# Kernel tuning notes

Measured on AMD Instinct MI355X. Metric: run time of the kernel, lower is better.

## Reference

```python
import jax, jax.numpy as jnp
import numpy as np

NUM_GRAPHS = 64

def _sage(x, edge_index, Wl, bl, Wr):
    # PyG SAGEConv (mean aggr): out = lin_l(mean_{j in N(i)} x_j) + lin_r(x_i)
    src, dst = edge_index[0], edge_index[1]
    n = x.shape[0]
    summed = jax.ops.segment_sum(x[src], dst, num_segments=n)        # [N,F]
    deg = jax.ops.segment_sum(jnp.ones_like(src, dtype=x.dtype), dst, num_segments=n)
    agg = summed / jnp.maximum(deg, 1.0)[:, None]
    return agg @ Wl.T + bl + x @ Wr.T

def setup_inputs() -> dict:
    key = jax.random.key(0)
    ks = jax.random.split(key, 12)
    N, E, F, H = 50000, 600000, 128, 128
    x = jax.random.normal(ks[0], (N, F), dtype=jnp.float32)
    edge_index = jax.random.randint(ks[1], (2, E), 0, N, dtype=jnp.int64)
    batch = jnp.sort(jax.random.randint(ks[2], (N,), 0, NUM_GRAPHS, dtype=jnp.int64))
    s = lambda fan_in: 1.0 / np.sqrt(fan_in)
    return {
        "x": x, "edge_index": edge_index, "batch": batch,
        "W1l": jax.random.uniform(ks[3], (H, F), minval=-s(F), maxval=s(F)),
        "b1l": jnp.zeros((H,), jnp.float32),
        "W1r": jax.random.uniform(ks[4], (H, F), minval=-s(F), maxval=s(F)),
        "W2l": jax.random.uniform(ks[5], (H, H), minval=-s(H), maxval=s(H)),
        "b2l": jnp.zeros((H,), jnp.float32),
        "W2r": jax.random.uniform(ks[6], (H, H), minval=-s(H), maxval=s(H)),
        "Wc1": jax.random.uniform(ks[7], (H, H), minval=-s(H), maxval=s(H)),
        "bc1": jax.random.uniform(ks[8], (H,), minval=-s(H), maxval=s(H)),
        "Wc2": jax.random.uniform(ks[9], (1, H), minval=-s(H), maxval=s(H)),
        "bc2": jax.random.uniform(ks[10], (1,), minval=-s(H), maxval=s(H)),
    }

def reference(x, edge_index, batch, W1l, b1l, W1r, W2l, b2l, W2r, Wc1, bc1, Wc2, bc2):
    h = jax.nn.relu(_sage(x, edge_index, W1l, b1l, W1r))
    h = jax.nn.relu(_sage(h, edge_index, W2l, b2l, W2r))
    # global mean pool per graph
    gsum = jax.ops.segment_sum(h, batch, num_segments=NUM_GRAPHS)
    gcnt = jax.ops.segment_sum(jnp.ones((h.shape[0],), h.dtype), batch, num_segments=NUM_GRAPHS)
    gemb = gsum / jnp.maximum(gcnt, 1.0)[:, None]                    # [G,H]
    # classifier MLP (dropout = identity in eval)
    z = jax.nn.relu(gemb @ Wc1.T + bc1)
    out = (z @ Wc2.T + bc2).squeeze(-1)                              # [G]
    return out
```

## Files before the change

### kernel.cpp

```cpp
#include <hip/hip_runtime.h>


typedef __attribute__((ext_vector_type(8))) short bf16x8;
typedef __attribute__((ext_vector_type(8))) unsigned short ushort8;
typedef __attribute__((ext_vector_type(4))) float f32x4;

#define HBLK 4096

__device__ inline unsigned short f2bf(float f) {
  unsigned u = __float_as_uint(f);
  u += 0x7fff + ((u >> 16) & 1);
  return (unsigned short)(u >> 16);
}
__device__ inline float bf2f(unsigned short h) { return __uint_as_float(((unsigned)h) << 16); }


__device__ inline void wprep_body(int id, const float* __restrict__ Wl, const float* __restrict__ Wr,
                                  unsigned short* __restrict__ Bpre) {
  if (id >= 4096) return;
  int kk = id >> 9;
  int ct = (id >> 6) & 7;
  int l  = id & 63;
  int colIdx = ct * 16 + (l & 15);
  int k0 = kk * 32 + (l >> 4) * 8;
  const float* W = (k0 < 128) ? Wl : Wr;
  int kb = k0 & 127;
#pragma unroll
  for (int j = 0; j < 8; ++j) {
    float v = W[colIdx * 128 + kb + j];
    unsigned short h = f2bf(v);
    size_t bh = (size_t)kk * 8192 + ((size_t)ct * 64 + l) * 8 + j;
    Bpre[bh] = h;
    Bpre[bh + 4096] = f2bf(v - bf2f(h));
  }
}

__global__ __launch_bounds__(256) void k_prep(
    const float* __restrict__ x, unsigned short* __restrict__ xbf, int total,
    const float* __restrict__ W1l, const float* __restrict__ W1r, unsigned short* __restrict__ Bpre1,
    const float* __restrict__ W2l, const float* __restrict__ W2r, unsigned short* __restrict__ Bpre2,
    const int* __restrict__ batch, int* __restrict__ gcnt, float* __restrict__ gsum, int N,
    const int* __restrict__ ei, int* __restrict__ bhist, int E,
    int nTobf, int nEblk) {
  __shared__ int h[256];
  int b = blockIdx.x;
  int tid = threadIdx.x;
  if (b < nTobf) {
    int i = (b * 256 + tid) * 4;
    if (i + 3 < total) {
      float4 v = *(const float4*)(x + i);
      ushort4 p;
      p.x = f2bf(v.x); p.y = f2bf(v.y); p.z = f2bf(v.z); p.w = f2bf(v.w);
      *(ushort4*)(xbf + i) = p;
    } else {
      for (int k = 0; k < 4 && i + k < total; ++k) xbf[i + k] = f2bf(x[i + k]);
    }
  } else if (b < nTobf + 16) {
    wprep_body((b - nTobf) * 256 + tid, W1l, W1r, Bpre1);
  } else if (b < nTobf + 32) {
    wprep_body((b - nTobf - 16) * 256 + tid, W2l, W2r, Bpre2);
  } else if (b < nTobf + 32 + nEblk) {
    int eb = b - nTobf - 32;
    h[tid] = 0;
    __syncthreads();
    int base = eb * HBLK;
    int end = min(base + HBLK, E);
    for (int e = base + tid; e < end; e += 256) atomicAdd(&h[ei[E + e] >> 8], 1);
    __syncthreads();
    bhist[eb * 256 + tid] = h[tid];
  } else {
    for (int i = tid; i < 64 * 128; i += 256) gsum[i] = 0.f;
    if (tid < 64) {
      int g = tid;
      int lo = 0, hi = N;
      while (lo < hi) { int mid = (lo + hi) >> 1; if (batch[mid] < g) lo = mid + 1; else hi = mid; }
      int a = lo;
      lo = 0; hi = N;
      while (lo < hi) { int mid = (lo + hi) >> 1; if (batch[mid] < g + 1) lo = mid + 1; else hi = mid; }
      gcnt[g] = lo - a;
    }
  }
}


__global__ __launch_bounds__(256) void k_bscan(int* __restrict__ bhist, int* __restrict__ bukbase,
                                               int nblk) {
  __shared__ int s[256];
  int buk = blockIdx.x;
  int t = threadIdx.x;
  int sum = 0;
  for (int b = 0; b < nblk; ++b) sum += bhist[b * 256 + t];
  s[t] = sum;
  __syncthreads();
  for (int d = 1; d < 256; d <<= 1) {
    int v = (t >= d) ? s[t - d] : 0;
    __syncthreads();
    s[t] += v;
    __syncthreads();
  }
  int myBase = (buk == 0) ? 0 : s[buk - 1];
  int tot = s[255];
  __syncthreads();
  int c = (t < nblk) ? bhist[t * 256 + buk] : 0;
  s[t] = c;
  __syncthreads();
  for (int d = 1; d < 256; d <<= 1) {
    int v = (t >= d) ? s[t - d] : 0;
    __syncthreads();
    s[t] += v;
    __syncthreads();
  }
  if (t < nblk) bhist[t * 256 + buk] = myBase + s[t] - c;
  if (t == 0) bukbase[buk] = myBase;
  if (buk == 255 && t == 1) bukbase[256] = tot;
}

__global__ __launch_bounds__(256) void k_scat(const int* __restrict__ ei, const int* __restrict__ bhist,
                                              unsigned* __restrict__ ebuk, int E) {
  __shared__ int cur[256];
  int tid = threadIdx.x;
  cur[tid] = bhist[blockIdx.x * 256 + tid];
  __syncthreads();
  int base = blockIdx.x * HBLK;
  int end = min(base + HBLK, E);
  for (int e = base + tid; e < end; e += 256) {
    int d = ei[E + e];
    int srcv = ei[e];
    int p = atomicAdd(&cur[d >> 8], 1);
    ebuk[p] = ((unsigned)(d & 255) << 24) | (unsigned)srcv;
  }
}

__global__ __launch_bounds__(256) void k_bucket(const unsigned* __restrict__ ebuk,
                                                const int* __restrict__ bukbase,
                                                int* __restrict__ off, int* __restrict__ colv,
                                                int N, int E) {
  __shared__ int h[256];
  __shared__ int cur[256];
  __shared__ int sc[256];
  int tid = threadIdx.x;
  int buk = blockIdx.x;
  int b0 = bukbase[buk], b1 = bukbase[buk + 1];
  h[tid] = 0;
  __syncthreads();
  for (int i = b0 + tid; i < b1; i += 256) atomicAdd(&h[ebuk[i] >> 24], 1);
  __syncthreads();
  int my = h[tid];
  sc[tid] = my;
  __syncthreads();
  for (int d = 1; d < 256; d <<= 1) {
    int v = (tid >= d) ? sc[tid - d] : 0;
    __syncthreads();
    sc[tid] += v;
    __syncthreads();
  }
  int excl = sc[tid] - my;
  cur[tid] = excl;
  int node = buk * 256 + tid;
  if (node < N) off[node] = b0 + excl;
  if (buk == gridDim.x - 1 && tid == 0) off[N] = E;
  __syncthreads();
  for (int i = b0 + tid; i < b1; i += 256) {
    unsigned v = ebuk[i];
    int p = atomicAdd(&cur[v >> 24], 1);
    colv[b0 + p] = (int)(v & 0xFFFFFFu);
  }
}


__global__ __launch_bounds__(256) void k_agg_bf(const unsigned short* __restrict__ Xbf,
                                                const int* __restrict__ off, const int* __restrict__ col,
                                                unsigned short* __restrict__ Tbf, int N) {
  int wid = (blockIdx.x * 256 + threadIdx.x) >> 6;
  int ln = threadIdx.x & 63;
  if (wid >= N) return;
  int o0 = off[wid], o1 = off[wid + 1];
  int deg = o1 - o0;
  int rs = ln >> 4, fs = ln & 15;
  float acc[8];
#pragma unroll
  for (int j = 0; j < 8; ++j) acc[j] = 0.f;

  for (int base = 0; base < deg; base += 16) {
#pragma unroll
    for (int u = 0; u < 4; ++u) {
      int n = base + u * 4 + rs;
      if (n < deg) {
        int idx = col[o0 + n];
        ushort8 q = *(const ushort8*)(Xbf + (size_t)idx * 128 + fs * 8);
#pragma unroll
        for (int j = 0; j < 8; ++j) acc[j] += bf2f(q[j]);
      }
    }
  }
#pragma unroll
  for (int j = 0; j < 8; ++j) {
    acc[j] += __shfl_xor(acc[j], 16);
    acc[j] += __shfl_xor(acc[j], 32);
  }
  if (rs == 0) {
    float sc = 1.0f / (float)max(deg, 1);
    unsigned short w[8];
#pragma unroll
    for (int j = 0; j < 8; ++j) w[j] = f2bf(acc[j] * sc);
    uint4 uw;
    uw.x = (unsigned)w[0] | ((unsigned)w[1] << 16);
    uw.y = (unsigned)w[2] | ((unsigned)w[3] << 16);
    uw.z = (unsigned)w[4] | ((unsigned)w[5] << 16);
    uw.w = (unsigned)w[6] | ((unsigned)w[7] << 16);
    *(uint4*)(Tbf + (size_t)wid * 128 + fs * 8) = uw;
  }
}


__global__ __launch_bounds__(256) void k_lin_mfma(
    const unsigned short* __restrict__ Agg,
    const unsigned short* __restrict__ Self,
    const unsigned short* __restrict__ Bpre,
    const float* __restrict__ bias,
    unsigned short* __restrict__ OUTbf,
    const int* __restrict__ batch, float* __restrict__ gsum,
    int N, int mode) {
  __shared__ unsigned short As[2048];
  __shared__ unsigned short Bs[8192];
  __shared__ float ps[128];

  int tid = threadIdx.x;
  int wv = tid >> 6, ln = tid & 63;
  int rowBase = blockIdx.x * 64;

  int sRow = tid >> 2;
  int sKq = tid & 3;
  int sgr = min(rowBase + sRow, N - 1);
  int sSlot = ((sRow >> 4) * 64 + (sKq << 4) + (sRow & 15)) * 8;

  f32x4 acc[4][2];
#pragma unroll
  for (int rg = 0; rg < 4; ++rg) {
    acc[rg][0] = (f32x4){0.f, 0.f, 0.f, 0.f};
    acc[rg][1] = (f32x4){0.f, 0.f, 0.f, 0.f};
  }

  const uint4* BpreV = (const uint4*)Bpre;

  for (int kk = 0; kk < 8; ++kk) {
    const unsigned short* S = (kk < 4) ? Agg : Self;
    int kOff = (kk & 3) * 32 + sKq * 8;
    uint4 ua = *(const uint4*)(S + (size_t)sgr * 128 + kOff);
    uint4 b0 = BpreV[kk * 1024 + tid];
    uint4 b1 = BpreV[kk * 1024 + tid + 256];
    uint4 b2 = BpreV[kk * 1024 + tid + 512];
    uint4 b3 = BpreV[kk * 1024 + tid + 768];

    __syncthreads();
    *(uint4*)(As + sSlot) = ua;
    uint4* BsV = (uint4*)Bs;
    BsV[tid] = b0;
    BsV[tid + 256] = b1;
    BsV[tid + 512] = b2;
    BsV[tid + 768] = b3;
    __syncthreads();

    int c0 = wv * 2;
    bf16x8 bh0 = *(bf16x8*)(Bs + ((size_t)c0 * 64 + ln) * 8);
    bf16x8 bl0 = *(bf16x8*)(Bs + 4096 + ((size_t)c0 * 64 + ln) * 8);
    bf16x8 bh1 = *(bf16x8*)(Bs + ((size_t)(c0 + 1) * 64 + ln) * 8);
    bf16x8 bl1 = *(bf16x8*)(Bs + 4096 + ((size_t)(c0 + 1) * 64 + ln) * 8);
#pragma unroll
    for (int rg = 0; rg < 4; ++rg) {
      bf16x8 ah = *(bf16x8*)(As + ((size_t)rg * 64 + ln) * 8);
      acc[rg][0] = __builtin_amdgcn_mfma_f32_16x16x32_bf16(ah, bh0, acc[rg][0], 0, 0, 0);
      acc[rg][0] = __builtin_amdgcn_mfma_f32_16x16x32_bf16(ah, bl0, acc[rg][0], 0, 0, 0);
      acc[rg][1] = __builtin_amdgcn_mfma_f32_16x16x32_bf16(ah, bh1, acc[rg][1], 0, 0, 0);
      acc[rg][1] = __builtin_amdgcn_mfma_f32_16x16x32_bf16(ah, bl1, acc[rg][1], 0, 0, 0);
    }
  }

  int lcol = ln & 15;
  int rsub = (ln >> 4) * 4;
#pragma unroll
  for (int c = 0; c < 2; ++c) {
    float b = bias[(wv * 2 + c) * 16 + lcol];
#pragma unroll
    for (int rg = 0; rg < 4; ++rg)
#pragma unroll
      for (int r = 0; r < 4; ++r) acc[rg][c][r] = fmaxf(acc[rg][c][r] + b, 0.f);
  }

  if (mode == 0) {
#pragma unroll
    for (int rg = 0; rg < 4; ++rg)
#pragma unroll
      for (int r = 0; r < 4; ++r) {
        int row = rowBase + rg * 16 + rsub + r;
        if (row < N) {
          OUTbf[(size_t)row * 128 + (wv * 2 + 0) * 16 + lcol] = f2bf(acc[rg][0][r]);
          OUTbf[(size_t)row * 128 + (wv * 2 + 1) * 16 + lcol] = f2bf(acc[rg][1][r]);
        }
      }
  } else {
    if (tid < 128) ps[tid] = 0.f;
    __syncthreads();
    int lastRow = min(rowBase + 63, N - 1);
    int g0 = batch[rowBase], g1 = batch[lastRow];
    if (g0 == g1) {
#pragma unroll
      for (int c = 0; c < 2; ++c) {
        float s = 0.f;
#pragma unroll
        for (int rg = 0; rg < 4; ++rg)
#pragma unroll
          for (int r = 0; r < 4; ++r) {
            int row = rowBase + rg * 16 + rsub + r;
            if (row < N) s += acc[rg][c][r];
          }
        atomicAdd(&ps[(wv * 2 + c) * 16 + lcol], s);
      }
      __syncthreads();
      if (tid < 128) atomicAdd(&gsum[g0 * 128 + tid], ps[tid]);
    } else {
#pragma unroll
      for (int rg = 0; rg < 4; ++rg)
#pragma unroll
        for (int r = 0; r < 4; ++r) {
          int row = rowBase + rg * 16 + rsub + r;
          if (row < N) {
            int g = batch[row];
            atomicAdd(&gsum[g * 128 + (wv * 2 + 0) * 16 + lcol], acc[rg][0][r]);
            atomicAdd(&gsum[g * 128 + (wv * 2 + 1) * 16 + lcol], acc[rg][1][r]);
          }
        }
    }
  }
}


__global__ __launch_bounds__(128) void k_cls(const float* __restrict__ gsum, const int* __restrict__ gcnt,
                                             const float* __restrict__ Wc1, const float* __restrict__ bc1,
                                             const float* __restrict__ Wc2, const float* __restrict__ bc2,
                                             float* __restrict__ out) {
  __shared__ float red[128];
  int g = blockIdx.x;
  int h = threadIdx.x;
  float inv = 1.0f / (float)max(gcnt[g], 1);
  float s = 0.f;
  for (int f = 0; f < 128; ++f) s += gsum[g * 128 + f] * Wc1[h * 128 + f];
  red[h] = fmaxf(s * inv + bc1[h], 0.f) * Wc2[h];
  __syncthreads();
  for (int d = 64; d > 0; d >>= 1) {
    if (h < d) red[h] += red[h + d];
    __syncthreads();
  }
  if (h == 0) out[g] = red[0] + bc2[0];
}


extern "C" void kernel_launch(void* const* d_in, const int* in_sizes, int n_in,
                              void* d_out, int out_size, void* d_ws, size_t ws_size,
                              hipStream_t stream) {
  const float* x   = (const float*)d_in[0];
  const int*   ei  = (const int*)d_in[1];
  const int*   bat = (const int*)d_in[2];
  const float* W1l = (const float*)d_in[3];
  const float* b1l = (const float*)d_in[4];
  const float* W1r = (const float*)d_in[5];
  const float* W2l = (const float*)d_in[6];
  const float* b2l = (const float*)d_in[7];
  const float* W2r = (const float*)d_in[8];
  const float* Wc1 = (const float*)d_in[9];
  const float* bc1 = (const float*)d_in[10];
  const float* Wc2 = (const float*)d_in[11];
  const float* bc2 = (const float*)d_in[12];
  float* out = (float*)d_out;

  int N = in_sizes[0] / 128;
  int E = in_sizes[1] / 2;
  int nEblk = (E + HBLK - 1) / HBLK;
  int nBuk = (N + 255) >> 8;
  int total = N * 128;
  int nTobf = (total / 4 + 255) / 256;

  char* ws = (char*)d_ws;
  size_t o = 0;
  auto alloc = [&](size_t bytes) {
    char* p = ws + o;
    o += (bytes + 255) & ~(size_t)255;
    return p;
  };
  int*      off    = (int*)alloc((size_t)(N + 1) * 4);
  int*      col    = (int*)alloc((size_t)E * 4);
  unsigned* ebuk   = (unsigned*)alloc((size_t)E * 4);
  int*      bhist  = (int*)alloc((size_t)nEblk * 256 * 4);
  int*      bukbase= (int*)alloc(257 * 4);
  unsigned short* Tbf  = (unsigned short*)alloc((size_t)N * 128 * 2);
  unsigned short* xbf  = (unsigned short*)alloc((size_t)N * 128 * 2);
  unsigned short* h1bf = (unsigned short*)alloc((size_t)N * 128 * 2);
  unsigned short* Bpre1 = (unsigned short*)alloc(65536 * 2);
  unsigned short* Bpre2 = (unsigned short*)alloc(65536 * 2);
  float*    gsum   = (float*)alloc(64 * 128 * 4 + 64 * 4);
  int*      gcnt   = (int*)(gsum + 64 * 128);

  k_prep<<<nTobf + 32 + nEblk + 1, 256, 0, stream>>>(
      x, xbf, total, W1l, W1r, Bpre1, W2l, W2r, Bpre2,
      bat, gcnt, gsum, N, ei, bhist, E, nTobf, nEblk);

  k_bscan<<<256, 256, 0, stream>>>(bhist, bukbase, nEblk);
  k_scat<<<nEblk, 256, 0, stream>>>(ei, bhist, ebuk, E);
  k_bucket<<<nBuk, 256, 0, stream>>>(ebuk, bukbase, off, col, N, E);

  int nLinBlk = (N + 63) / 64;
  k_agg_bf<<<(N + 3) / 4, 256, 0, stream>>>(xbf, off, col, Tbf, N);
  k_lin_mfma<<<nLinBlk, 256, 0, stream>>>(Tbf, xbf, Bpre1, b1l, h1bf, bat, gsum, N, 0);
  k_agg_bf<<<(N + 3) / 4, 256, 0, stream>>>(h1bf, off, col, Tbf, N);
  k_lin_mfma<<<nLinBlk, 256, 0, stream>>>(Tbf, h1bf, Bpre2, b2l, nullptr, bat, gsum, N, 1);

  k_cls<<<64, 128, 0, stream>>>(gsum, gcnt, Wc1, bc1, Wc2, bc2, out);
}
```

Baseline: 163.6 us.

## Fold bucket scan into scatter and bucket kernels, widen aggregation unroll

Removes the separate k_bscan launch. Each k_scat block now recomputes the column sums of the block histogram, scans them for bucket bases, and adds its own prefix over earlier blocks. k_bucket recomputes the same scan to get its bucket range. This trades one kernel launch and its global round-trip for redundant histogram reads in every block (nblk×256 ints, about 147 blocks). Separately, the aggregation loop is unrolled to 8 neighbour groups per iteration to expose more memory-level parallelism.

```diff
diff --git a/kernel.cpp b/kernel.cpp
--- a/kernel.cpp
+++ b/kernel.cpp
@@ -83,14 +83,19 @@
 }
 
 
-__global__ __launch_bounds__(256) void k_bscan(int* __restrict__ bhist, int* __restrict__ bukbase,
-                                               int nblk) {
+__global__ __launch_bounds__(256) void k_scat(const int* __restrict__ ei, const int* __restrict__ bhist,
+                                              unsigned* __restrict__ ebuk, int E, int nblk) {
+  __shared__ int cur[256];
   __shared__ int s[256];
-  int buk = blockIdx.x;
   int t = threadIdx.x;
-  int sum = 0;
-  for (int b = 0; b < nblk; ++b) sum += bhist[b * 256 + t];
-  s[t] = sum;
+  int b = blockIdx.x;
+  int colsum = 0, mypre = 0;
+  for (int i = 0; i < nblk; ++i) {
+    int v = bhist[i * 256 + t];
+    colsum += v;
+    if (i < b) mypre += v;
+  }
+  s[t] = colsum;
   __syncthreads();
   for (int d = 1; d < 256; d <<= 1) {
     int v = (t >= d) ? s[t - d] : 0;
@@ -98,32 +103,11 @@
     s[t] += v;
     __syncthreads();
   }
-  int myBase = (buk == 0) ? 0 : s[buk - 1];
-  int tot = s[255];
-  __syncthreads();
-  int c = (t < nblk) ? bhist[t * 256 + buk] : 0;
-  s[t] = c;
-  __syncthreads();
-  for (int d = 1; d < 256; d <<= 1) {
-    int v = (t >= d) ? s[t - d] : 0;
-    __syncthreads();
-    s[t] += v;
-    __syncthreads();
-  }
-  if (t < nblk) bhist[t * 256 + buk] = myBase + s[t] - c;
-  if (t == 0) bukbase[buk] = myBase;
-  if (buk == 255 && t == 1) bukbase[256] = tot;
-}
-
-__global__ __launch_bounds__(256) void k_scat(const int* __restrict__ ei, const int* __restrict__ bhist,
-                                              unsigned* __restrict__ ebuk, int E) {
-  __shared__ int cur[256];
-  int tid = threadIdx.x;
-  cur[tid] = bhist[blockIdx.x * 256 + tid];
-  __syncthreads();
-  int base = blockIdx.x * HBLK;
+  cur[t] = (s[t] - colsum) + mypre;
+  __syncthreads();
+  int base = b * HBLK;
   int end = min(base + HBLK, E);
-  for (int e = base + tid; e < end; e += 256) {
+  for (int e = base + t; e < end; e += 256) {
     int d = ei[E + e];
     int srcv = ei[e];
     int p = atomicAdd(&cur[d >> 8], 1);
@@ -132,15 +116,31 @@
 }
 
 __global__ __launch_bounds__(256) void k_bucket(const unsigned* __restrict__ ebuk,
-                                                const int* __restrict__ bukbase,
+                                                const int* __restrict__ bhist,
                                                 int* __restrict__ off, int* __restrict__ colv,
-                                                int N, int E) {
+                                                int N, int E, int nblk) {
   __shared__ int h[256];
   __shared__ int cur[256];
   __shared__ int sc[256];
+  __shared__ int bb[2];
   int tid = threadIdx.x;
   int buk = blockIdx.x;
-  int b0 = bukbase[buk], b1 = bukbase[buk + 1];
+  int colsum = 0;
+  for (int i = 0; i < nblk; ++i) colsum += bhist[i * 256 + tid];
+  sc[tid] = colsum;
+  __syncthreads();
+  for (int d = 1; d < 256; d <<= 1) {
+    int v = (tid >= d) ? sc[tid - d] : 0;
+    __syncthreads();
+    sc[tid] += v;
+    __syncthreads();
+  }
+  if (tid == buk) {
+    bb[0] = sc[buk] - colsum;
+    bb[1] = sc[buk];
+  }
+  __syncthreads();
+  int b0 = bb[0], b1 = bb[1];
   h[tid] = 0;
   __syncthreads();
   for (int i = b0 + tid; i < b1; i += 256) atomicAdd(&h[ebuk[i] >> 24], 1);
@@ -181,9 +181,9 @@
 #pragma unroll
   for (int j = 0; j < 8; ++j) acc[j] = 0.f;
 
-  for (int base = 0; base < deg; base += 16) {
-#pragma unroll
-    for (int u = 0; u < 4; ++u) {
+  for (int base = 0; base < deg; base += 32) {
+#pragma unroll
+    for (int u = 0; u < 8; ++u) {
       int n = base + u * 4 + rs;
       if (n < deg) {
         int idx = col[o0 + n];
@@ -391,7 +391,6 @@
   int*      col    = (int*)alloc((size_t)E * 4);
   unsigned* ebuk   = (unsigned*)alloc((size_t)E * 4);
   int*      bhist  = (int*)alloc((size_t)nEblk * 256 * 4);
-  int*      bukbase= (int*)alloc(257 * 4);
   unsigned short* Tbf  = (unsigned short*)alloc((size_t)N * 128 * 2);
   unsigned short* xbf  = (unsigned short*)alloc((size_t)N * 128 * 2);
   unsigned short* h1bf = (unsigned short*)alloc((size_t)N * 128 * 2);
@@ -404,9 +403,8 @@
       x, xbf, total, W1l, W1r, Bpre1, W2l, W2r, Bpre2,
       bat, gcnt, gsum, N, ei, bhist, E, nTobf, nEblk);
 
-  k_bscan<<<256, 256, 0, stream>>>(bhist, bukbase, nEblk);
-  k_scat<<<nEblk, 256, 0, stream>>>(ei, bhist, ebuk, E);
-  k_bucket<<<nBuk, 256, 0, stream>>>(ebuk, bukbase, off, col, N, E);
+  k_scat<<<nEblk, 256, 0, stream>>>(ei, bhist, ebuk, E, nEblk);
+  k_bucket<<<nBuk, 256, 0, stream>>>(ebuk, bhist, off, col, N, E, nEblk);
 
   int nLinBlk = (N + 63) / 64;
   k_agg_bf<<<(N + 3) / 4, 256, 0, stream>>>(xbf, off, col, Tbf, N);
```

New measurement: 171.0 us. 4.5% more time.
